# Kernel optimization log

Hardware: AMD Instinct MI355X
Metric: run time of the kernel (lower is better)

## Reference

```python
import jax, jax.numpy as jnp
import numpy as np

N_NODES = 50000
N_EDGES = 500000
D_IN = 128
HID = 128
N_GRAPHS = 256


def setup_inputs() -> dict:
    key = jax.random.key(0)
    ks = jax.random.split(key, 10)
    x = jax.random.normal(ks[0], (N_NODES, D_IN), dtype=jnp.float32)
    edge_index = jax.random.randint(ks[1], (2, N_EDGES), 0, N_NODES, dtype=jnp.int64)
    batch = jnp.sort(jax.random.randint(ks[2], (N_NODES,), 0, N_GRAPHS, dtype=jnp.int64))
    s = 1.0 / np.sqrt(D_IN)
    W1_rel = jax.random.uniform(ks[3], (HID, D_IN), jnp.float32, -s, s)
    W1_root = jax.random.uniform(ks[4], (HID, D_IN), jnp.float32, -s, s)
    b1 = jnp.zeros((HID,), jnp.float32)
    s2 = 1.0 / np.sqrt(HID)
    W2_rel = jax.random.uniform(ks[5], (HID, HID), jnp.float32, -s2, s2)
    W2_root = jax.random.uniform(ks[6], (HID, HID), jnp.float32, -s2, s2)
    b2 = jnp.zeros((HID,), jnp.float32)
    W_out = jax.random.uniform(ks[7], (1, HID), jnp.float32, -s2, s2)
    b_out = jnp.zeros((1,), jnp.float32)
    return {"x": x, "edge_index": edge_index, "batch": batch,
            "W1_rel": W1_rel, "W1_root": W1_root, "b1": b1,
            "W2_rel": W2_rel, "W2_root": W2_root, "b2": b2,
            "W_out": W_out, "b_out": b_out}


def _graph_conv(h, src, dst, W_rel, W_root, b):
    # gather neighbor feats at edge sources, sum-aggregate at destinations
    agg = jax.ops.segment_sum(h[src], dst, num_segments=N_NODES)  # [N, d]
    return agg @ W_rel.T + h @ W_root.T + b


def reference(x, edge_index, batch, W1_rel, W1_root, b1, W2_rel, W2_root, b2, W_out, b_out):
    src, dst = edge_index[0], edge_index[1]
    h = jax.nn.relu(_graph_conv(x, src, dst, W1_rel, W1_root, b1))
    h = jax.nn.relu(_graph_conv(h, src, dst, W2_rel, W2_root, b2))
    # global mean pool per graph
    sums = jax.ops.segment_sum(h, batch, num_segments=N_GRAPHS)  # [G, HID]
    cnts = jax.ops.segment_sum(jnp.ones((N_NODES,), h.dtype), batch, num_segments=N_GRAPHS)
    pooled = sums / jnp.maximum(cnts, 1.0)[:, None]
    return pooled @ W_out.T + b_out  # [G, 1]
```

## Files before the change

kernel.cpp:

```cpp
#include <hip/hip_runtime.h>
#include <hip/hip_bf16.h>

#define N_NODES  50000
#define N_EDGES  500000
#define DIM      128
#define N_GRAPHS 256

#define SCAN_B   512
#define SCAN_NB  ((N_NODES + SCAN_B - 1) / SCAN_B)

#define PB_CVT   6250
#define PB_W     32
#define PB_DEG   ((N_NODES + 255) / 256)
#define PB_POOL  128
#define PB_TOTAL (PB_CVT + PB_W + PB_DEG + PB_POOL)

typedef __attribute__((ext_vector_type(8))) short bf16x8;
typedef __attribute__((ext_vector_type(4))) float f32x4;

__device__ __forceinline__ unsigned short f2bf(float f) {
    __hip_bfloat16 h = __float2bfloat16(f);
    return *(unsigned short*)&h;
}
__device__ __forceinline__ float bflo(unsigned int v) { return __uint_as_float(v << 16); }
__device__ __forceinline__ float bfhi(unsigned int v) { return __uint_as_float(v & 0xffff0000u); }

__global__ __launch_bounds__(256)
void prep_kernel(const float* __restrict__ x,
                 const float* __restrict__ W1_rel, const float* __restrict__ W1_root,
                 const float* __restrict__ W2_rel, const float* __restrict__ W2_root,
                 unsigned short* __restrict__ xb, unsigned short* __restrict__ Wb,
                 int* __restrict__ deg, float* __restrict__ pooled)
{
    int b = blockIdx.x, t = threadIdx.x;
    if (b < PB_CVT) {
        int i = b * 256 + t;
        float4 v = ((const float4*)x)[i];
        ushort4 o;
        o.x = f2bf(v.x); o.y = f2bf(v.y); o.z = f2bf(v.z); o.w = f2bf(v.w);
        ((ushort4*)xb)[i] = o;
    } else if (b < PB_CVT + PB_W) {
        int u = (b - PB_CVT) * 256 + t;
        int layer = u >> 12;
        int kb    = (u >> 7) & 31;
        int col   = u & 127;
        int k0    = kb * 8;
        const float* Wrel  = layer ? W2_rel  : W1_rel;
        const float* Wroot = layer ? W2_root : W1_root;
        const float* srcp = (k0 < 128) ? (Wrel + col * 128 + k0)
                                       : (Wroot + col * 128 + (k0 - 128));
        float4 v0 = ((const float4*)srcp)[0];
        float4 v1 = ((const float4*)srcp)[1];
        ushort4 o0, o1;
        o0.x = f2bf(v0.x); o0.y = f2bf(v0.y); o0.z = f2bf(v0.z); o0.w = f2bf(v0.w);
        o1.x = f2bf(v1.x); o1.y = f2bf(v1.y); o1.z = f2bf(v1.z); o1.w = f2bf(v1.w);
        unsigned short* dst = Wb + (size_t)layer * 32768 + ((kb * 128 + col) * 8);
        ((ushort4*)dst)[0] = o0;
        ((ushort4*)dst)[1] = o1;
    } else if (b < PB_CVT + PB_W + PB_DEG) {
        int i = (b - PB_CVT - PB_W) * 256 + t;
        if (i < N_NODES) deg[i] = 0;
    } else {
        int i = (b - PB_CVT - PB_W - PB_DEG) * 256 + t;
        pooled[i] = 0.f;
    }
}

__global__ void hist_kernel(const int* __restrict__ dst, int* __restrict__ deg)
{
    int e = blockIdx.x * blockDim.x + threadIdx.x;
    if (e < N_EDGES) atomicAdd(&deg[dst[e]], 1);
}

__global__ __launch_bounds__(SCAN_B)
void block_sum_kernel(const int* __restrict__ deg, int* __restrict__ bsum)
{
    __shared__ int red[SCAN_B];
    int t = threadIdx.x;
    int idx = blockIdx.x * SCAN_B + t;
    red[t] = (idx < N_NODES) ? deg[idx] : 0;
    __syncthreads();
    for (int off = SCAN_B / 2; off > 0; off >>= 1) {
        if (t < off) red[t] += red[t + off];
        __syncthreads();
    }
    if (t == 0) bsum[blockIdx.x] = red[0];
}

__global__ __launch_bounds__(128)
void scan_sums_kernel(int* __restrict__ bsum)
{
    __shared__ int s[128];
    int t = threadIdx.x;
    int v = (t < SCAN_NB) ? bsum[t] : 0;
    s[t] = v;
    __syncthreads();
    for (int off = 1; off < 128; off <<= 1) {
        int u = (t >= off) ? s[t - off] : 0;
        __syncthreads();
        s[t] += u;
        __syncthreads();
    }
    if (t < SCAN_NB) bsum[t] = s[t] - v;
}

__global__ __launch_bounds__(SCAN_B)
void scan_apply_kernel(const int* __restrict__ deg, const int* __restrict__ bsum,
                       int* __restrict__ row_ptr, int* __restrict__ cursor)
{
    __shared__ int s[SCAN_B];
    int t = threadIdx.x;
    int idx = blockIdx.x * SCAN_B + t;
    int v = (idx < N_NODES) ? deg[idx] : 0;
    s[t] = v;
    __syncthreads();
    for (int off = 1; off < SCAN_B; off <<= 1) {
        int u = (t >= off) ? s[t - off] : 0;
        __syncthreads();
        s[t] += u;
        __syncthreads();
    }
    if (idx < N_NODES) {
        int ex = bsum[blockIdx.x] + s[t] - v;
        row_ptr[idx] = ex;
        cursor[idx]  = ex;
    }
    if (idx == 0) row_ptr[N_NODES] = N_EDGES;
}

__global__ void build_kernel(const int* __restrict__ src, const int* __restrict__ dst,
                             int* __restrict__ cursor, int* __restrict__ edge_src)
{
    int e = blockIdx.x * blockDim.x + threadIdx.x;
    if (e < N_EDGES) {
        int pos = atomicAdd(&cursor[dst[e]], 1);
        edge_src[pos] = src[e];
    }
}

__global__ __launch_bounds__(256)
void gather_kernel(const unsigned short* __restrict__ feat,
                   const int* __restrict__ row_ptr,
                   const int* __restrict__ edge_src,
                   unsigned short* __restrict__ agg)
{
    int wid  = (blockIdx.x * blockDim.x + threadIdx.x) >> 6;
    int lane = threadIdx.x & 63;
    int node = __builtin_amdgcn_readfirstlane(wid);
    int half = lane >> 5;
    int l31  = lane & 31;

    const uint2* f = (const uint2*)feat;
    int e  = row_ptr[node];
    int e1 = row_ptr[node + 1];

    float a0 = 0.f, a1 = 0.f, a2 = 0.f, a3 = 0.f;
    float b0 = 0.f, b1 = 0.f, b2 = 0.f, b3 = 0.f;

    for (; e + 7 < e1; e += 8) {
#pragma unroll
        for (int p = 0; p < 4; ++p) {
            int idx = edge_src[e + p * 2 + half];
            uint2 v = f[idx * 32 + l31];
            if (p & 1) {
                b0 += bflo(v.x); b1 += bfhi(v.x); b2 += bflo(v.y); b3 += bfhi(v.y);
            } else {
                a0 += bflo(v.x); a1 += bfhi(v.x); a2 += bflo(v.y); a3 += bfhi(v.y);
            }
        }
    }
    for (; e < e1; e += 2) {
        int my = e + half;
        if (my < e1) {
            uint2 v = f[edge_src[my] * 32 + l31];
            a0 += bflo(v.x); a1 += bfhi(v.x); a2 += bflo(v.y); a3 += bfhi(v.y);
        }
    }
    a0 += b0; a1 += b1; a2 += b2; a3 += b3;
    a0 += __shfl_xor(a0, 32, 64);
    a1 += __shfl_xor(a1, 32, 64);
    a2 += __shfl_xor(a2, 32, 64);
    a3 += __shfl_xor(a3, 32, 64);
    if (half == 0) {
        uint2 o;
        o.x = (unsigned)f2bf(a0) | ((unsigned)f2bf(a1) << 16);
        o.y = (unsigned)f2bf(a2) | ((unsigned)f2bf(a3) << 16);
        ((uint2*)agg)[node * 32 + l31] = o;
    }
}

template <bool POOL>
__global__ __launch_bounds__(256)
void gemm_mfma(const unsigned short* __restrict__ Aagg,
               const unsigned short* __restrict__ Ax,
               const unsigned short* __restrict__ Wb,
               const float* __restrict__ bias,
               unsigned short* __restrict__ Hout,
               float* __restrict__ pooled,
               const int* __restrict__ batch)
{
    __shared__ __align__(16) unsigned short wlds[32768];

    const int t = threadIdx.x;

    {
        const uint4* s4 = (const uint4*)Wb;
        uint4* d4 = (uint4*)wlds;
#pragma unroll
        for (int i = 0; i < 16; ++i) d4[t + i * 256] = s4[t + i * 256];
    }
    __syncthreads();

    const int wave = t >> 6;
    const int lane = t & 63;
    const int q    = lane >> 4;
    const int ln15 = lane & 15;
    const int m0   = blockIdx.x * 128 + wave * 16;

    int r0 = m0 + ln15;      int r0c = r0 < N_NODES ? r0 : N_NODES - 1;
    int r1 = m0 + 64 + ln15; int r1c = r1 < N_NODES ? r1 : N_NODES - 1;

    const unsigned short* A00 = Aagg + (size_t)r0c * DIM + q * 8;
    const unsigned short* A01 = Ax   + (size_t)r0c * DIM + q * 8;
    const unsigned short* A10 = Aagg + (size_t)r1c * DIM + q * 8;
    const unsigned short* A11 = Ax   + (size_t)r1c * DIM + q * 8;

    f32x4 acc0[8], acc1[8];
#pragma unroll
    for (int ct = 0; ct < 8; ++ct) {
        acc0[ct] = (f32x4){0.f, 0.f, 0.f, 0.f};
        acc1[ct] = (f32x4){0.f, 0.f, 0.f, 0.f};
    }

#pragma unroll
    for (int ks = 0; ks < 8; ++ks) {
        const unsigned short* p0 = (ks < 4) ? (A00 + ks * 32) : (A01 + (ks - 4) * 32);
        const unsigned short* p1 = (ks < 4) ? (A10 + ks * 32) : (A11 + (ks - 4) * 32);
        bf16x8 a0 = *(const bf16x8*)p0;
        bf16x8 a1 = *(const bf16x8*)p1;
        const unsigned short* wrow = wlds + (ks * 4 + q) * 1024;
#pragma unroll
        for (int ct = 0; ct < 8; ++ct) {
            bf16x8 bf = *(const bf16x8*)&wrow[(ct * 16 + ln15) * 8];
            acc0[ct] = __builtin_amdgcn_mfma_f32_16x16x32_bf16(a0, bf, acc0[ct], 0, 0, 0);
            acc1[ct] = __builtin_amdgcn_mfma_f32_16x16x32_bf16(a1, bf, acc1[ct], 0, 0, 0);
        }
    }

    float bj[8];
#pragma unroll
    for (int ct = 0; ct < 8; ++ct) bj[ct] = bias[ct * 16 + ln15];

#pragma unroll
    for (int rt = 0; rt < 2; ++rt) {
        const f32x4* acc = rt ? acc1 : acc0;
        const int rb = m0 + rt * 64 + q * 4;

        if (!POOL) {
#pragma unroll
            for (int ct = 0; ct < 8; ++ct) {
                int coln = ct * 16 + ln15;
#pragma unroll
                for (int r = 0; r < 4; ++r) {
                    int row = rb + r;
                    if (row < N_NODES) {
                        float v = acc[ct][r] + bj[ct];
                        v = v > 0.f ? v : 0.f;
                        Hout[(size_t)row * DIM + coln] = f2bf(v);
                    }
                }
            }
        } else {
            int gg[4];
#pragma unroll
            for (int r = 0; r < 4; ++r) gg[r] = (rb + r < N_NODES) ? batch[rb + r] : -1;
            bool uni = (gg[0] == gg[3]) && (gg[3] >= 0);
#pragma unroll
            for (int ct = 0; ct < 8; ++ct) {
                int coln = ct * 16 + ln15;
                float v[4];
#pragma unroll
                for (int r = 0; r < 4; ++r) {
                    float x = acc[ct][r] + bj[ct];
                    v[r] = x > 0.f ? x : 0.f;
                }
                if (uni) {
                    atomicAdd(&pooled[gg[0] * DIM + coln], v[0] + v[1] + v[2] + v[3]);
                } else {
#pragma unroll
                    for (int r = 0; r < 4; ++r)
                        if (gg[r] >= 0) atomicAdd(&pooled[gg[r] * DIM + coln], v[r]);
                }
            }
        }
    }
}

__global__ void finalize_kernel(const float* __restrict__ pooled, const int* __restrict__ batch,
                                const float* __restrict__ Wout, const float* __restrict__ bout,
                                float* __restrict__ out)
{
    int g = blockIdx.x;
    int lane = threadIdx.x;

    int lo0 = 0, hi0 = N_NODES;
    while (lo0 < hi0) { int m = (lo0 + hi0) >> 1; if (batch[m] < g) lo0 = m + 1; else hi0 = m; }
    int lo1 = lo0, hi1 = N_NODES;
    while (lo1 < hi1) { int m = (lo1 + hi1) >> 1; if (batch[m] < g + 1) lo1 = m + 1; else hi1 = m; }
    int cnt = lo1 - lo0;

    float s = pooled[g * DIM + lane]      * Wout[lane]
            + pooled[g * DIM + 64 + lane] * Wout[64 + lane];
#pragma unroll
    for (int off = 32; off > 0; off >>= 1) s += __shfl_xor(s, off, 64);
    if (lane == 0) {
        float c = (float)(cnt > 1 ? cnt : 1);
        out[g] = s / c + bout[0];
    }
}

extern "C" void kernel_launch(void* const* d_in, const int* in_sizes, int n_in,
                              void* d_out, int out_size, void* d_ws, size_t ws_size,
                              hipStream_t stream)
{
    const float* x       = (const float*)d_in[0];
    const int*   ei      = (const int*)d_in[1];
    const int*   batch   = (const int*)d_in[2];
    const float* W1_rel  = (const float*)d_in[3];
    const float* W1_root = (const float*)d_in[4];
    const float* b1      = (const float*)d_in[5];
    const float* W2_rel  = (const float*)d_in[6];
    const float* W2_root = (const float*)d_in[7];
    const float* b2      = (const float*)d_in[8];
    const float* W_out   = (const float*)d_in[9];
    const float* b_out   = (const float*)d_in[10];
    float* out = (float*)d_out;

    const int* src  = ei;
    const int* dstv = ei + N_EDGES;

    char* ws = (char*)d_ws;
    unsigned short* aggb = (unsigned short*)ws;
    unsigned short* xb   = (unsigned short*)(ws + 12800000);
    unsigned short* h1b  = (unsigned short*)(ws + 25600000);
    float* pooled        = (float*)(ws + 38400000);
    int*   deg           = (int*)  (ws + 38531072);
    int*   row_ptr       = (int*)  (ws + 38731072);
    int*   edge_src      = (int*)  (ws + 38931200);
    int*   cursor        = (int*)  (ws + 40931200);
    int*   bsum          = (int*)  (ws + 41131200);
    unsigned short* Wb   = (unsigned short*)(ws + 41131712);

    prep_kernel      <<<PB_TOTAL, 256, 0, stream>>>(x, W1_rel, W1_root, W2_rel, W2_root,
                                                    xb, Wb, deg, pooled);
    hist_kernel      <<<(N_EDGES + 255) / 256, 256, 0, stream>>>(dstv, deg);
    block_sum_kernel <<<SCAN_NB, SCAN_B, 0, stream>>>(deg, bsum);
    scan_sums_kernel <<<1, 128, 0, stream>>>(bsum);
    scan_apply_kernel<<<SCAN_NB, SCAN_B, 0, stream>>>(deg, bsum, row_ptr, cursor);
    build_kernel     <<<(N_EDGES + 255) / 256, 256, 0, stream>>>(src, dstv, cursor, edge_src);

    const int gemm_grid = (N_NODES + 127) / 128;

    gather_kernel<<<N_NODES / 4, 256, 0, stream>>>(xb, row_ptr, edge_src, aggb);
    gemm_mfma<false><<<gemm_grid, 256, 0, stream>>>(
        aggb, xb, Wb, b1, h1b, nullptr, nullptr);

    gather_kernel<<<N_NODES / 4, 256, 0, stream>>>(h1b, row_ptr, edge_src, aggb);
    gemm_mfma<true><<<gemm_grid, 256, 0, stream>>>(
        aggb, h1b, Wb + 32768, b2, nullptr, pooled, batch);

    finalize_kernel<<<N_GRAPHS, 64, 0, stream>>>(pooled, batch, W_out, b_out, out);
}
```

Baseline: 242.8 us.

## Fuse three-kernel scan into chained single-pass scan; read GEMM weights from global

Replaces the block-sum, sum-scan and apply kernels with one chained-scan kernel. Each block spins on its predecessor's flag to get its running prefix, which removes two kernel launches and their serialization gaps. The GEMM kernel also stops staging the 64KB weight tile in LDS and reads weights directly from global/L2. That removes the per-block copy and barrier, and the large LDS footprint that limited occupancy. The costs are serialized spin-waiting across ~98 scan blocks, which relies on blocks being scheduled in order, and uncached-by-LDS repeated weight loads that go through L1/L2.

```diff
diff --git a/kernel.cpp b/kernel.cpp
--- a/kernel.cpp
+++ b/kernel.cpp
@@ -13,7 +13,8 @@
 #define PB_W     32
 #define PB_DEG   ((N_NODES + 255) / 256)
 #define PB_POOL  128
-#define PB_TOTAL (PB_CVT + PB_W + PB_DEG + PB_POOL)
+#define PB_FLAG  1
+#define PB_TOTAL (PB_CVT + PB_W + PB_DEG + PB_POOL + PB_FLAG)
 
 typedef __attribute__((ext_vector_type(8))) short bf16x8;
 typedef __attribute__((ext_vector_type(4))) float f32x4;
@@ -30,7 +31,8 @@
                  const float* __restrict__ W1_rel, const float* __restrict__ W1_root,
                  const float* __restrict__ W2_rel, const float* __restrict__ W2_root,
                  unsigned short* __restrict__ xb, unsigned short* __restrict__ Wb,
-                 int* __restrict__ deg, float* __restrict__ pooled)
+                 int* __restrict__ deg, float* __restrict__ pooled,
+                 int* __restrict__ flags)
 {
     int b = blockIdx.x, t = threadIdx.x;
     if (b < PB_CVT) {
@@ -60,9 +62,11 @@
     } else if (b < PB_CVT + PB_W + PB_DEG) {
         int i = (b - PB_CVT - PB_W) * 256 + t;
         if (i < N_NODES) deg[i] = 0;
-    } else {
+    } else if (b < PB_CVT + PB_W + PB_DEG + PB_POOL) {
         int i = (b - PB_CVT - PB_W - PB_DEG) * 256 + t;
         pooled[i] = 0.f;
+    } else {
+        if (t < SCAN_NB) flags[t] = 0;
     }
 }
 
@@ -73,44 +77,13 @@
 }
 
 __global__ __launch_bounds__(SCAN_B)
-void block_sum_kernel(const int* __restrict__ deg, int* __restrict__ bsum)
-{
-    __shared__ int red[SCAN_B];
-    int t = threadIdx.x;
-    int idx = blockIdx.x * SCAN_B + t;
-    red[t] = (idx < N_NODES) ? deg[idx] : 0;
-    __syncthreads();
-    for (int off = SCAN_B / 2; off > 0; off >>= 1) {
-        if (t < off) red[t] += red[t + off];
-        __syncthreads();
-    }
-    if (t == 0) bsum[blockIdx.x] = red[0];
-}
-
-__global__ __launch_bounds__(128)
-void scan_sums_kernel(int* __restrict__ bsum)
-{
-    __shared__ int s[128];
-    int t = threadIdx.x;
-    int v = (t < SCAN_NB) ? bsum[t] : 0;
-    s[t] = v;
-    __syncthreads();
-    for (int off = 1; off < 128; off <<= 1) {
-        int u = (t >= off) ? s[t - off] : 0;
-        __syncthreads();
-        s[t] += u;
-        __syncthreads();
-    }
-    if (t < SCAN_NB) bsum[t] = s[t] - v;
-}
-
-__global__ __launch_bounds__(SCAN_B)
-void scan_apply_kernel(const int* __restrict__ deg, const int* __restrict__ bsum,
+void scan_chain_kernel(const int* __restrict__ deg, int* __restrict__ bflags,
                        int* __restrict__ row_ptr, int* __restrict__ cursor)
 {
     __shared__ int s[SCAN_B];
-    int t = threadIdx.x;
-    int idx = blockIdx.x * SCAN_B + t;
+    __shared__ int base_s;
+    int b = blockIdx.x, t = threadIdx.x;
+    int idx = b * SCAN_B + t;
     int v = (idx < N_NODES) ? deg[idx] : 0;
     s[t] = v;
     __syncthreads();
@@ -120,8 +93,19 @@
         s[t] += u;
         __syncthreads();
     }
+    if (t == 0) {
+        int base = 0;
+        if (b > 0) {
+            int f;
+            while ((f = atomicAdd(&bflags[b - 1], 0)) == 0) { __builtin_amdgcn_s_sleep(1); }
+            base = f - 1;
+        }
+        atomicExch(&bflags[b], base + s[SCAN_B - 1] + 1);
+        base_s = base;
+    }
+    __syncthreads();
     if (idx < N_NODES) {
-        int ex = bsum[blockIdx.x] + s[t] - v;
+        int ex = base_s + s[t] - v;
         row_ptr[idx] = ex;
         cursor[idx]  = ex;
     }
@@ -199,18 +183,7 @@
                float* __restrict__ pooled,
                const int* __restrict__ batch)
 {
-    __shared__ __align__(16) unsigned short wlds[32768];
-
-    const int t = threadIdx.x;
-
-    {
-        const uint4* s4 = (const uint4*)Wb;
-        uint4* d4 = (uint4*)wlds;
-#pragma unroll
-        for (int i = 0; i < 16; ++i) d4[t + i * 256] = s4[t + i * 256];
-    }
-    __syncthreads();
-
+    const int t    = threadIdx.x;
     const int wave = t >> 6;
     const int lane = t & 63;
     const int q    = lane >> 4;
@@ -225,6 +198,8 @@
     const unsigned short* A10 = Aagg + (size_t)r1c * DIM + q * 8;
     const unsigned short* A11 = Ax   + (size_t)r1c * DIM + q * 8;
 
+    const unsigned short* Wl = Wb + q * 1024 + ln15 * 8;
+
     f32x4 acc0[8], acc1[8];
 #pragma unroll
     for (int ct = 0; ct < 8; ++ct) {
@@ -234,14 +209,12 @@
 
 #pragma unroll
     for (int ks = 0; ks < 8; ++ks) {
-        const unsigned short* p0 = (ks < 4) ? (A00 + ks * 32) : (A01 + (ks - 4) * 32);
-        const unsigned short* p1 = (ks < 4) ? (A10 + ks * 32) : (A11 + (ks - 4) * 32);
-        bf16x8 a0 = *(const bf16x8*)p0;
-        bf16x8 a1 = *(const bf16x8*)p1;
-        const unsigned short* wrow = wlds + (ks * 4 + q) * 1024;
+        bf16x8 a0 = *(const bf16x8*)((ks < 4) ? (A00 + ks * 32) : (A01 + (ks - 4) * 32));
+        bf16x8 a1 = *(const bf16x8*)((ks < 4) ? (A10 + ks * 32) : (A11 + (ks - 4) * 32));
+        const unsigned short* wk = Wl + ks * 4096;
 #pragma unroll
         for (int ct = 0; ct < 8; ++ct) {
-            bf16x8 bf = *(const bf16x8*)&wrow[(ct * 16 + ln15) * 8];
+            bf16x8 bf = *(const bf16x8*)(wk + ct * 128);
             acc0[ct] = __builtin_amdgcn_mfma_f32_16x16x32_bf16(a0, bf, acc0[ct], 0, 0, 0);
             acc1[ct] = __builtin_amdgcn_mfma_f32_16x16x32_bf16(a1, bf, acc1[ct], 0, 0, 0);
         }
@@ -348,15 +321,13 @@
     int*   row_ptr       = (int*)  (ws + 38731072);
     int*   edge_src      = (int*)  (ws + 38931200);
     int*   cursor        = (int*)  (ws + 40931200);
-    int*   bsum          = (int*)  (ws + 41131200);
+    int*   flags         = (int*)  (ws + 41131200);
     unsigned short* Wb   = (unsigned short*)(ws + 41131712);
 
     prep_kernel      <<<PB_TOTAL, 256, 0, stream>>>(x, W1_rel, W1_root, W2_rel, W2_root,
-                                                    xb, Wb, deg, pooled);
+                                                    xb, Wb, deg, pooled, flags);
     hist_kernel      <<<(N_EDGES + 255) / 256, 256, 0, stream>>>(dstv, deg);
-    block_sum_kernel <<<SCAN_NB, SCAN_B, 0, stream>>>(deg, bsum);
-    scan_sums_kernel <<<1, 128, 0, stream>>>(bsum);
-    scan_apply_kernel<<<SCAN_NB, SCAN_B, 0, stream>>>(deg, bsum, row_ptr, cursor);
+    scan_chain_kernel<<<SCAN_NB, SCAN_B, 0, stream>>>(deg, flags, row_ptr, cursor);
     build_kernel     <<<(N_EDGES + 255) / 256, 256, 0, stream>>>(src, dstv, cursor, edge_src);
 
     const int gemm_grid = (N_NODES + 127) / 128;
```

Result: slower. 303.2 us (+24.9%).
